# Performance work log

Measured on AMD Instinct MI355X. Metric: run time of the kernel, lower is better.

## Reference

```python
import jax, jax.numpy as jnp
import numpy as np

B, N, DIM = 4, 2048, 512
H, DH = 8, 64  # heads, dim_head; inner_dim = H*DH = 512


def setup_inputs() -> dict:
    key = jax.random.key(0)
    ks = jax.random.split(key, 7)
    s = 0.02
    return {
        "x": jax.random.normal(ks[0], (B, N, DIM), dtype=jnp.float32),
        "w_qkv": jax.random.normal(ks[1], (DIM, 3 * H * DH), dtype=jnp.float32) * s,
        "b_qkv": jnp.zeros((3 * H * DH,), dtype=jnp.float32),
        "th1": jax.random.normal(ks[2], (H, H), dtype=jnp.float32) * (1.0 / H) + jnp.eye(H, dtype=jnp.float32),
        "th2": jax.random.normal(ks[3], (H, H), dtype=jnp.float32) * (1.0 / H) + jnp.eye(H, dtype=jnp.float32),
        "w_out": jax.random.normal(ks[4], (H * DH, DIM), dtype=jnp.float32) * s,
        "b_out": jnp.zeros((DIM,), dtype=jnp.float32),
    }


def reference(x, w_qkv, b_qkv, th1, th2, w_out, b_out):
    b, n, _ = x.shape
    scale = DH ** -0.5
    qkv = x @ w_qkv + b_qkv                       # [b, n, 3*H*DH]
    q, k, v = jnp.split(qkv, 3, axis=-1)
    to_heads = lambda t: t.reshape(b, n, H, DH).transpose(0, 2, 1, 3)  # b h n d
    q, k, v = to_heads(q), to_heads(k), to_heads(v)
    dots = jnp.einsum('bhnd,bhmd->bhnm', q, k) * scale   # [b, h, n, n]
    dots = jnp.einsum('gh,bhnm->bgnm', th1, dots)        # talking-heads pre-softmax (1x1 conv over heads)
    attn = jax.nn.softmax(dots, axis=-1)
    attn = jnp.einsum('gh,bhnm->bgnm', th2, attn)        # talking-heads post-softmax
    out = jnp.einsum('bhnm,bhmd->bhnd', attn, v)         # [b, h, n, d]
    out = out.transpose(0, 2, 1, 3).reshape(b, n, H * DH)
    return out @ w_out + b_out
```

## Files before the change

kernel.cpp:

```cpp
#include <hip/hip_runtime.h>

typedef _Float16 half8  __attribute__((ext_vector_type(8)));
typedef _Float16 half4  __attribute__((ext_vector_type(4)));
typedef float    f32x4  __attribute__((ext_vector_type(4)));

#define MFMA32(a,b,c) __builtin_amdgcn_mfma_f32_16x16x32_f16(a,b,c,0,0,0)
#define MFMA16(a,b,c) __builtin_amdgcn_mfma_f32_16x16x16f16(a,b,c,0,0,0)

#if __has_builtin(__builtin_amdgcn_exp2f)
#define EXP2F(x) __builtin_amdgcn_exp2f(x)
#else
#define EXP2F(x) exp2f(x)
#endif

#define GLOAD16(gp, lp) __builtin_amdgcn_global_load_lds(                      \
    (const __attribute__((address_space(1))) void*)(gp),                       \
    (__attribute__((address_space(3))) void*)(lp), 16, 0, 0)

static constexpr float SCALE_LOG2E = 0.18033688011112042f;

static constexpr size_t QH_OFF = 0;
static constexpr size_t KH_OFF = (size_t)8  << 20;
static constexpr size_t VT_OFF = (size_t)16 << 20;
static constexpr size_t LS_OFF = (size_t)24 << 20;
static constexpr size_t O_OFF  = (size_t)25 << 20;
static constexpr size_t LPART  = (size_t)4*8*2048;
static constexpr size_t OPART  = (size_t)8192*512;

__global__ __launch_bounds__(256)
void k_qkv(const float* __restrict__ x, const float* __restrict__ w,
           const float* __restrict__ bias, _Float16* __restrict__ Qh,
           _Float16* __restrict__ Kh, _Float16* __restrict__ Vt)
{
  __shared__ __align__(16) _Float16 Xs[64*40];
  __shared__ __align__(16) _Float16 Wt[64*40];
  const int tid = threadIdx.x;
  const int wv = tid >> 6, lane = tid & 63, l15 = lane & 15, qd = lane >> 4;
  const int row0 = blockIdx.x * 64, col0 = blockIdx.y * 64;

  const int xr = tid >> 2, xc = (tid & 3) * 8;
  const int wk = tid >> 3, wc = (tid & 7) * 8;

  f32x4 acc[4] = {{0.f,0.f,0.f,0.f},{0.f,0.f,0.f,0.f},{0.f,0.f,0.f,0.f},{0.f,0.f,0.f,0.f}};

  for (int k0 = 0; k0 < 512; k0 += 32) {
    f32x4 a0 = *(const f32x4*)(x + (size_t)(row0 + xr) * 512 + k0 + xc);
    f32x4 a1 = *(const f32x4*)(x + (size_t)(row0 + xr) * 512 + k0 + xc + 4);
    f32x4 b0 = *(const f32x4*)(w + (size_t)(k0 + wk) * 1536 + col0 + wc);
    f32x4 b1 = *(const f32x4*)(w + (size_t)(k0 + wk) * 1536 + col0 + wc + 4);
    half8 hx;
#pragma unroll
    for (int j = 0; j < 4; j++) { hx[j] = (_Float16)a0[j]; hx[j+4] = (_Float16)a1[j]; }
    *(half8*)&Xs[xr*40 + xc] = hx;
#pragma unroll
    for (int j = 0; j < 4; j++) {
      Wt[(wc+j  )*40 + wk] = (_Float16)b0[j];
      Wt[(wc+j+4)*40 + wk] = (_Float16)b1[j];
    }
    __syncthreads();
    half8 af = *(const half8*)&Xs[(wv*16 + l15)*40 + qd*8];
#pragma unroll
    for (int ct = 0; ct < 4; ct++) {
      half8 bf = *(const half8*)&Wt[(ct*16 + l15)*40 + qd*8];
      acc[ct] = MFMA32(af, bf, acc[ct]);
    }
    __syncthreads();
  }
#pragma unroll
  for (int ct = 0; ct < 4; ct++) {
    const int c = col0 + ct*16 + l15;
    const int sec = c >> 9, hh = (c >> 6) & 7, d = c & 63;
    const float bv = bias[c];
#pragma unroll
    for (int i = 0; i < 4; i++) {
      const int row = row0 + wv*16 + qd*4 + i;
      const int bb = row >> 11, n = row & 2047;
      float v = acc[ct][i] + bv;
      if (sec == 0)
        Qh[((size_t)((bb*8 + hh)*2048 + n))*64 + d] = (_Float16)(v * SCALE_LOG2E);
      else if (sec == 1)
        Kh[((size_t)((bb*8 + hh)*2048 + n))*64 + d] = (_Float16)v;
      else
        Vt[((size_t)((bb*8 + hh)*64 + d))*2048 + n] = (_Float16)v;
    }
  }
}

__global__ __launch_bounds__(512, 4)
void k_pass1(const _Float16* __restrict__ Qh, const _Float16* __restrict__ Kh,
             const float* __restrict__ th1, float* __restrict__ Lsum)
{
  __shared__ __align__(16) _Float16 KB[8][1024];
  __shared__ __align__(16) _Float16 Sb[2][2][2592];
  const int tid = threadIdx.x;
  const int wv = tid >> 6, lane = tid & 63, l15 = lane & 15, qd = lane >> 4;
  const int s = blockIdx.x & 7, nt = blockIdx.x >> 3;
  const int b = s >> 1, mh = s & 1;
  const int n0 = nt << 5;
  const _Float16* kbase = Kh + ((size_t)((b*8 + wv)*2048 + mh*1024))*64;

  half4 a1f;
#pragma unroll
  for (int j = 0; j < 4; j++)
    a1f[j] = ((l15 >> 3) == (qd >> 1)) ? (_Float16)th1[(l15 & 7)*8 + (qd & 1)*4 + j]
                                       : (_Float16)0.f;

  half8 qf[2][2];
#pragma unroll
  for (int t = 0; t < 2; t++) {
    const _Float16* qp = Qh + ((size_t)((b*8 + wv)*2048 + n0 + t*16 + l15))*64 + qd*8;
    qf[t][0] = *(const half8*)qp;
    qf[t][1] = *(const half8*)(qp + 32);
  }

  auto issueK = [&](int it) {
#pragma unroll
    for (int j = 0; j < 2; j++) {
      const int bk = j*64 + lane;
      const int m = bk >> 3, c = bk & 7;
      const int cp = c ^ (m & 7);
      GLOAD16(kbase + (size_t)(it*16 + m)*64 + cp*8, &KB[wv][j*512]);
    }
  };
  auto qk_to_sb = [&](int buf) {
    half8 ka0 = *(const half8*)&KB[wv][l15*64 + ((qd       ^ (l15 & 7))*8)];
    half8 ka1 = *(const half8*)&KB[wv][l15*64 + (((4 + qd) ^ (l15 & 7))*8)];
#pragma unroll
    for (int t = 0; t < 2; t++) {
      f32x4 a = {0.f,0.f,0.f,0.f};
      a = MFMA32(ka0, qf[t][0], a);
      a = MFMA32(ka1, qf[t][1], a);
#pragma unroll
      for (int i = 0; i < 4; i++)
        Sb[buf][t][(l15 >> 1)*324 + (qd*4 + i)*20 + wv + 8*(l15 & 1)] = (_Float16)a[i];
    }
  };

  float lacc[2][4];
#pragma unroll
  for (int t = 0; t < 2; t++)
#pragma unroll
    for (int i = 0; i < 4; i++) lacc[t][i] = 0.f;

  issueK(0);
  __syncthreads();
  for (int it = 0; it <= 64; it++) {
    if (it < 64) {
      qk_to_sb(it & 1);
      if (it + 1 < 64) issueK(it + 1);
    }
    if (it >= 1) {
      const int buf = (it - 1) & 1;
#pragma unroll
      for (int t = 0; t < 2; t++) {
        half4 b1 = *(const half4*)&Sb[buf][t][wv*324 + l15*20 + qd*4];
        f32x4 c1 = MFMA16(a1f, b1, ((f32x4){0.f,0.f,0.f,0.f}));
#pragma unroll
        for (int i = 0; i < 4; i++) lacc[t][i] += EXP2F(c1[i]);
      }
    }
    __syncthreads();
  }

#pragma unroll
  for (int t = 0; t < 2; t++)
#pragma unroll
    for (int i = 0; i < 4; i++) {
      float v = lacc[t][i];
      v += __shfl_xor(v, 1); v += __shfl_xor(v, 2);
      v += __shfl_xor(v, 4); v += __shfl_xor(v, 8);
      lacc[t][i] = v;
    }
  if (l15 == 0) {
#pragma unroll
    for (int t = 0; t < 2; t++)
#pragma unroll
      for (int i = 0; i < 4; i++) {
        const int n = n0 + t*16 + wv*2 + (qd >> 1);
        const int g = (qd & 1)*4 + i;
        Lsum[(size_t)mh*LPART + (size_t)(b*8 + g)*2048 + n] = lacc[t][i];
      }
  }
}

__global__ __launch_bounds__(512, 4)
void k_pass2(const _Float16* __restrict__ Qh, const _Float16* __restrict__ Kh,
             const _Float16* __restrict__ Vt, const float* __restrict__ Lsum,
             const float* __restrict__ th1, const float* __restrict__ th2,
             _Float16* __restrict__ Obuf)
{
  __shared__ __align__(16) _Float16 KB[8][1024];
  __shared__ __align__(16) _Float16 VB[8][1024];
  __shared__ __align__(16) _Float16 Sb[2][2][2592];
  __shared__ __align__(16) _Float16 Wb[2][2][2592];
  const int tid = threadIdx.x;
  const int wv = tid >> 6, lane = tid & 63, l15 = lane & 15, qd = lane >> 4;
  const int s = blockIdx.x & 7, nt = blockIdx.x >> 3;
  const int b = s >> 1, mh = s & 1;
  const int n0 = nt << 5;
  const _Float16* kbase = Kh + ((size_t)((b*8 + wv)*2048 + mh*1024))*64;
  const _Float16* vbase = Vt + (size_t)(b*8 + wv)*64*2048 + mh*1024;

  half4 a1f, b2f;
#pragma unroll
  for (int j = 0; j < 4; j++) {
    const bool diag = ((l15 >> 3) == (qd >> 1));
    a1f[j] = diag ? (_Float16)th1[(l15 & 7)*8 + (qd & 1)*4 + j] : (_Float16)0.f;
    b2f[j] = diag ? (_Float16)th2[(l15 & 7)*8 + (qd & 1)*4 + j] : (_Float16)0.f;
  }

  f32x4 cs[2];
#pragma unroll
  for (int t = 0; t < 2; t++)
#pragma unroll
    for (int i = 0; i < 4; i++) {
      const int n = n0 + t*16 + wv*2 + (qd >> 1);
      const int g = (qd & 1)*4 + i;
      const size_t off = (size_t)(b*8 + g)*2048 + n;
      cs[t][i] = -__log2f(Lsum[off] + Lsum[off + LPART]);
    }

  half8 qf[2][2];
#pragma unroll
  for (int t = 0; t < 2; t++) {
    const _Float16* qp = Qh + ((size_t)((b*8 + wv)*2048 + n0 + t*16 + l15))*64 + qd*8;
    qf[t][0] = *(const half8*)qp;
    qf[t][1] = *(const half8*)(qp + 32);
  }

  auto issueK = [&](int it) {
#pragma unroll
    for (int j = 0; j < 2; j++) {
      const int bk = j*64 + lane;
      const int m = bk >> 3, c = bk & 7;
      const int cp = c ^ (m & 7);
      GLOAD16(kbase + (size_t)(it*16 + m)*64 + cp*8, &KB[wv][j*512]);
    }
  };
  auto issueV = [&](int it) {
#pragma unroll
    for (int j = 0; j < 2; j++) {
      const int bk = j*64 + lane;
      const int d = bk >> 1, c = bk & 1;
      const int cp = c ^ ((d >> 2) & 1);
      GLOAD16(vbase + (size_t)d*2048 + it*16 + cp*8, &VB[wv][j*512]);
    }
  };
  auto qk_to_sb = [&](int buf) {
    half8 ka0 = *(const half8*)&KB[wv][l15*64 + ((qd       ^ (l15 & 7))*8)];
    half8 ka1 = *(const half8*)&KB[wv][l15*64 + (((4 + qd) ^ (l15 & 7))*8)];
#pragma unroll
    for (int t = 0; t < 2; t++) {
      f32x4 a = {0.f,0.f,0.f,0.f};
      a = MFMA32(ka0, qf[t][0], a);
      a = MFMA32(ka1, qf[t][1], a);
#pragma unroll
      for (int i = 0; i < 4; i++)
        Sb[buf][t][(l15 >> 1)*324 + (qd*4 + i)*20 + wv + 8*(l15 & 1)] = (_Float16)a[i];
    }
  };

  f32x4 og[2][4];
#pragma unroll
  for (int t = 0; t < 2; t++)
#pragma unroll
    for (int dt = 0; dt < 4; dt++)
      og[t][dt] = (f32x4){0.f,0.f,0.f,0.f};

  issueK(0);
  __syncthreads();

  for (int it = 0; it <= 65; it++) {
    if (it < 64) {
      qk_to_sb(it & 1);
      if (it + 1 < 64) issueK(it + 1);
    }
    if (it >= 1 && it <= 64) {
      const int buf = (it - 1) & 1;
#pragma unroll
      for (int t = 0; t < 2; t++) {
        half4 b1 = *(const half4*)&Sb[buf][t][wv*324 + l15*20 + qd*4];
        f32x4 c1 = MFMA16(a1f, b1, cs[t]);
        half4 a2;
#pragma unroll
        for (int i = 0; i < 4; i++) a2[i] = (_Float16)EXP2F(c1[i]);
        f32x4 c2 = MFMA16(a2, b2f, ((f32x4){0.f,0.f,0.f,0.f}));
        half4 w4;
#pragma unroll
        for (int i = 0; i < 4; i++) w4[i] = (_Float16)c2[i];
        *(half4*)&Wb[buf][t][(l15 & 7)*324 + (wv*2 + (l15 >> 3))*20 + qd*4] = w4;
      }
    }
    if (it >= 2) {
      const int buf = (it - 2) & 1;
      half4 vb[4];
#pragma unroll
      for (int dt = 0; dt < 4; dt++) {
        const int rv = dt*16 + l15;
        vb[dt] = *(const half4*)&VB[wv][rv*16 +
                  (((qd >> 1) ^ ((rv >> 2) & 1))*8) + (qd & 1)*4];
      }
#pragma unroll
      for (int t = 0; t < 2; t++) {
        half4 af = *(const half4*)&Wb[buf][t][wv*324 + l15*20 + qd*4];
#pragma unroll
        for (int dt = 0; dt < 4; dt++)
          og[t][dt] = MFMA16(af, vb[dt], og[t][dt]);
      }
    }
    if (it >= 1 && it <= 64) issueV(it - 1);
    __syncthreads();
  }

  _Float16* Op = Obuf + (size_t)mh * OPART + ((size_t)(b*2048 + n0))*512;
#pragma unroll
  for (int t = 0; t < 2; t++)
#pragma unroll
    for (int dt = 0; dt < 4; dt++)
#pragma unroll
      for (int i = 0; i < 4; i++)
        Op[(size_t)(t*16 + qd*4 + i)*512 + wv*64 + dt*16 + l15] = (_Float16)og[t][dt][i];
}

__global__ __launch_bounds__(256)
void k_oproj(const _Float16* __restrict__ Ob, const float* __restrict__ w,
             const float* __restrict__ bias, float* __restrict__ out)
{
  __shared__ __align__(16) _Float16 Xs[64*40];
  __shared__ __align__(16) _Float16 Wt[64*40];
  const int tid = threadIdx.x;
  const int wv = tid >> 6, lane = tid & 63, l15 = lane & 15, qd = lane >> 4;
  const int row0 = blockIdx.x * 64, col0 = blockIdx.y * 64;
  const int xr = tid >> 2, xc = (tid & 3) * 8;
  const int wk = tid >> 3, wc = (tid & 7) * 8;

  f32x4 acc[4] = {{0.f,0.f,0.f,0.f},{0.f,0.f,0.f,0.f},{0.f,0.f,0.f,0.f},{0.f,0.f,0.f,0.f}};

  for (int k0 = 0; k0 < 512; k0 += 32) {
    const size_t idx = (size_t)(row0 + xr)*512 + k0 + xc;
    half8 a0 = *(const half8*)(Ob + idx);
    half8 a1 = *(const half8*)(Ob + OPART + idx);
    *(half8*)&Xs[xr*40 + xc] = a0 + a1;
    f32x4 b0 = *(const f32x4*)(w + (size_t)(k0 + wk)*512 + col0 + wc);
    f32x4 b1 = *(const f32x4*)(w + (size_t)(k0 + wk)*512 + col0 + wc + 4);
#pragma unroll
    for (int j = 0; j < 4; j++) {
      Wt[(wc+j  )*40 + wk] = (_Float16)b0[j];
      Wt[(wc+j+4)*40 + wk] = (_Float16)b1[j];
    }
    __syncthreads();
    half8 af = *(const half8*)&Xs[(wv*16 + l15)*40 + qd*8];
#pragma unroll
    for (int ct = 0; ct < 4; ct++) {
      half8 bf = *(const half8*)&Wt[(ct*16 + l15)*40 + qd*8];
      acc[ct] = MFMA32(af, bf, acc[ct]);
    }
    __syncthreads();
  }
#pragma unroll
  for (int ct = 0; ct < 4; ct++) {
    const int c = col0 + ct*16 + l15;
    const float bv = bias[c];
#pragma unroll
    for (int i = 0; i < 4; i++) {
      const int row = row0 + wv*16 + qd*4 + i;
      out[(size_t)row*512 + c] = acc[ct][i] + bv;
    }
  }
}

extern "C" void kernel_launch(void* const* d_in, const int* in_sizes, int n_in,
                              void* d_out, int out_size, void* d_ws, size_t ws_size,
                              hipStream_t stream)
{
  (void)in_sizes; (void)n_in; (void)out_size;
  const float* x     = (const float*)d_in[0];
  const float* w_qkv = (const float*)d_in[1];
  const float* b_qkv = (const float*)d_in[2];
  const float* th1   = (const float*)d_in[3];
  const float* th2   = (const float*)d_in[4];
  const float* w_out = (const float*)d_in[5];
  const float* b_out = (const float*)d_in[6];
  float* out = (float*)d_out;

  char* ws = (char*)d_ws;
  _Float16* Qh   = (_Float16*)(ws + QH_OFF);
  _Float16* Kh   = (_Float16*)(ws + KH_OFF);
  _Float16* Vt   = (_Float16*)(ws + VT_OFF);
  float*    Lsum = (float*)   (ws + LS_OFF);
  _Float16* Obuf = (_Float16*)(ws + O_OFF);
  if (ws_size < ((size_t)41 << 20)) return;

  k_qkv  <<<dim3(128, 24), 256, 0, stream>>>(x, w_qkv, b_qkv, Qh, Kh, Vt);
  k_pass1<<<dim3(512),     512, 0, stream>>>(Qh, Kh, th1, Lsum);
  k_pass2<<<dim3(512),     512, 0, stream>>>(Qh, Kh, Vt, Lsum, th1, th2, Obuf);
  k_oproj<<<dim3(128, 8),  256, 0, stream>>>(Obuf, w_out, b_out, out);
}
```

Before: 351.9 us.

## Pre-convert x and transposed W to fp16 and stage QKV GEMM via async LDS loads

Adds two small kernels that convert x to fp16 and transpose-convert w_qkv to fp16. The QKV GEMM then loads its tiles with global_load_lds into XOR-swizzled shared memory instead of converting fp32 in registers, which removes the scalar transposed shared-memory stores. Separately, the attention kernels change the S/W staging stride from 324 to 340 and use a simpler unswizzled V tile layout. This adds two launches and extra global traffic for the converted copies, and the new stride and V layout may change bank-conflict behaviour.

```diff
diff --git a/kernel.cpp b/kernel.cpp
--- a/kernel.cpp
+++ b/kernel.cpp
@@ -27,41 +27,61 @@
 static constexpr size_t LPART  = (size_t)4*8*2048;
 static constexpr size_t OPART  = (size_t)8192*512;
 
+static constexpr int GS = 340;
+
 __global__ __launch_bounds__(256)
-void k_qkv(const float* __restrict__ x, const float* __restrict__ w,
+void k_cvtx(const float* __restrict__ x, _Float16* __restrict__ xf)
+{
+  const size_t i = ((size_t)blockIdx.x*256 + threadIdx.x)*4;
+  f32x4 v = *(const f32x4*)(x + i);
+  half4 h;
+#pragma unroll
+  for (int j = 0; j < 4; j++) h[j] = (_Float16)v[j];
+  *(half4*)(xf + i) = h;
+}
+
+__global__ __launch_bounds__(256)
+void k_cvtw(const float* __restrict__ w, _Float16* __restrict__ wt)
+{
+  __shared__ _Float16 T[32][36];
+  const int kt = blockIdx.x, ct = blockIdx.y;
+  const int r = threadIdx.x >> 3, c4 = (threadIdx.x & 7)*4;
+  f32x4 v = *(const f32x4*)(w + (size_t)(kt*32 + r)*1536 + ct*32 + c4);
+#pragma unroll
+  for (int j = 0; j < 4; j++) T[r][c4 + j] = (_Float16)v[j];
+  __syncthreads();
+  half4 o;
+#pragma unroll
+  for (int j = 0; j < 4; j++) o[j] = T[c4 + j][r];
+  *(half4*)(wt + (size_t)(ct*32 + r)*512 + kt*32 + c4) = o;
+}
+
+__global__ __launch_bounds__(256)
+void k_qkv(const _Float16* __restrict__ xf, const _Float16* __restrict__ wt,
            const float* __restrict__ bias, _Float16* __restrict__ Qh,
            _Float16* __restrict__ Kh, _Float16* __restrict__ Vt)
 {
-  __shared__ __align__(16) _Float16 Xs[64*40];
-  __shared__ __align__(16) _Float16 Wt[64*40];
+  __shared__ __align__(16) _Float16 Xs[2048];
+  __shared__ __align__(16) _Float16 Ws[2048];
   const int tid = threadIdx.x;
   const int wv = tid >> 6, lane = tid & 63, l15 = lane & 15, qd = lane >> 4;
   const int row0 = blockIdx.x * 64, col0 = blockIdx.y * 64;
 
-  const int xr = tid >> 2, xc = (tid & 3) * 8;
-  const int wk = tid >> 3, wc = (tid & 7) * 8;
+  const int sslot = wv*64 + lane;
+  const int sr = sslot >> 2, so = (sslot & 3) ^ ((sr >> 1) & 3);
 
   f32x4 acc[4] = {{0.f,0.f,0.f,0.f},{0.f,0.f,0.f,0.f},{0.f,0.f,0.f,0.f},{0.f,0.f,0.f,0.f}};
 
   for (int k0 = 0; k0 < 512; k0 += 32) {
-    f32x4 a0 = *(const f32x4*)(x + (size_t)(row0 + xr) * 512 + k0 + xc);
-    f32x4 a1 = *(const f32x4*)(x + (size_t)(row0 + xr) * 512 + k0 + xc + 4);
-    f32x4 b0 = *(const f32x4*)(w + (size_t)(k0 + wk) * 1536 + col0 + wc);
-    f32x4 b1 = *(const f32x4*)(w + (size_t)(k0 + wk) * 1536 + col0 + wc + 4);
-    half8 hx;
-#pragma unroll
-    for (int j = 0; j < 4; j++) { hx[j] = (_Float16)a0[j]; hx[j+4] = (_Float16)a1[j]; }
-    *(half8*)&Xs[xr*40 + xc] = hx;
-#pragma unroll
-    for (int j = 0; j < 4; j++) {
-      Wt[(wc+j  )*40 + wk] = (_Float16)b0[j];
-      Wt[(wc+j+4)*40 + wk] = (_Float16)b1[j];
-    }
-    __syncthreads();
-    half8 af = *(const half8*)&Xs[(wv*16 + l15)*40 + qd*8];
+    GLOAD16(xf + (size_t)(row0 + sr)*512 + k0 + so*8, &Xs[wv*512]);
+    GLOAD16(wt + (size_t)(col0 + sr)*512 + k0 + so*8, &Ws[wv*512]);
+    __syncthreads();
+    const int ra = wv*16 + l15;
+    half8 af = *(const half8*)&Xs[(ra*4 + (qd ^ ((ra >> 1) & 3)))*8];
 #pragma unroll
     for (int ct = 0; ct < 4; ct++) {
-      half8 bf = *(const half8*)&Wt[(ct*16 + l15)*40 + qd*8];
+      const int rb = ct*16 + l15;
+      half8 bf = *(const half8*)&Ws[(rb*4 + (qd ^ ((rb >> 1) & 3)))*8];
       acc[ct] = MFMA32(af, bf, acc[ct]);
     }
     __syncthreads();
@@ -91,7 +111,7 @@
              const float* __restrict__ th1, float* __restrict__ Lsum)
 {
   __shared__ __align__(16) _Float16 KB[8][1024];
-  __shared__ __align__(16) _Float16 Sb[2][2][2592];
+  __shared__ __align__(16) _Float16 Sb[2][2][2704];
   const int tid = threadIdx.x;
   const int wv = tid >> 6, lane = tid & 63, l15 = lane & 15, qd = lane >> 4;
   const int s = blockIdx.x & 7, nt = blockIdx.x >> 3;
@@ -132,7 +152,7 @@
       a = MFMA32(ka1, qf[t][1], a);
 #pragma unroll
       for (int i = 0; i < 4; i++)
-        Sb[buf][t][(l15 >> 1)*324 + (qd*4 + i)*20 + wv + 8*(l15 & 1)] = (_Float16)a[i];
+        Sb[buf][t][(l15 >> 1)*GS + (qd*4 + i)*20 + wv + 8*(l15 & 1)] = (_Float16)a[i];
     }
   };
 
@@ -153,7 +173,7 @@
       const int buf = (it - 1) & 1;
 #pragma unroll
       for (int t = 0; t < 2; t++) {
-        half4 b1 = *(const half4*)&Sb[buf][t][wv*324 + l15*20 + qd*4];
+        half4 b1 = *(const half4*)&Sb[buf][t][wv*GS + l15*20 + qd*4];
         f32x4 c1 = MFMA16(a1f, b1, ((f32x4){0.f,0.f,0.f,0.f}));
 #pragma unroll
         for (int i = 0; i < 4; i++) lacc[t][i] += EXP2F(c1[i]);
@@ -191,8 +211,8 @@
 {
   __shared__ __align__(16) _Float16 KB[8][1024];
   __shared__ __align__(16) _Float16 VB[8][1024];
-  __shared__ __align__(16) _Float16 Sb[2][2][2592];
-  __shared__ __align__(16) _Float16 Wb[2][2][2592];
+  __shared__ __align__(16) _Float16 Sb[2][2][2704];
+  __shared__ __align__(16) _Float16 Wb[2][2][2704];
   const int tid = threadIdx.x;
   const int wv = tid >> 6, lane = tid & 63, l15 = lane & 15, qd = lane >> 4;
   const int s = blockIdx.x & 7, nt = blockIdx.x >> 3;
@@ -239,12 +259,8 @@
   };
   auto issueV = [&](int it) {
 #pragma unroll
-    for (int j = 0; j < 2; j++) {
-      const int bk = j*64 + lane;
-      const int d = bk >> 1, c = bk & 1;
-      const int cp = c ^ ((d >> 2) & 1);
-      GLOAD16(vbase + (size_t)d*2048 + it*16 + cp*8, &VB[wv][j*512]);
-    }
+    for (int j = 0; j < 2; j++)
+      GLOAD16(vbase + (size_t)lane*2048 + it*16 + j*8, &VB[wv][j*512]);
   };
   auto qk_to_sb = [&](int buf) {
     half8 ka0 = *(const half8*)&KB[wv][l15*64 + ((qd       ^ (l15 & 7))*8)];
@@ -256,7 +272,7 @@
       a = MFMA32(ka1, qf[t][1], a);
 #pragma unroll
       for (int i = 0; i < 4; i++)
-        Sb[buf][t][(l15 >> 1)*324 + (qd*4 + i)*20 + wv + 8*(l15 & 1)] = (_Float16)a[i];
+        Sb[buf][t][(l15 >> 1)*GS + (qd*4 + i)*20 + wv + 8*(l15 & 1)] = (_Float16)a[i];
     }
   };
 
@@ -279,7 +295,7 @@
       const int buf = (it - 1) & 1;
 #pragma unroll
       for (int t = 0; t < 2; t++) {
-        half4 b1 = *(const half4*)&Sb[buf][t][wv*324 + l15*20 + qd*4];
+        half4 b1 = *(const half4*)&Sb[buf][t][wv*GS + l15*20 + qd*4];
         f32x4 c1 = MFMA16(a1f, b1, cs[t]);
         half4 a2;
 #pragma unroll
@@ -288,21 +304,18 @@
         half4 w4;
 #pragma unroll
         for (int i = 0; i < 4; i++) w4[i] = (_Float16)c2[i];
-        *(half4*)&Wb[buf][t][(l15 & 7)*324 + (wv*2 + (l15 >> 3))*20 + qd*4] = w4;
+        *(half4*)&Wb[buf][t][(l15 & 7)*GS + (wv*2 + (l15 >> 3))*20 + qd*4] = w4;
       }
     }
     if (it >= 2) {
       const int buf = (it - 2) & 1;
       half4 vb[4];
 #pragma unroll
-      for (int dt = 0; dt < 4; dt++) {
-        const int rv = dt*16 + l15;
-        vb[dt] = *(const half4*)&VB[wv][rv*16 +
-                  (((qd >> 1) ^ ((rv >> 2) & 1))*8) + (qd & 1)*4];
-      }
+      for (int dt = 0; dt < 4; dt++)
+        vb[dt] = *(const half4*)&VB[wv][((qd >> 1)*64 + dt*16 + l15)*8 + (qd & 1)*4];
 #pragma unroll
       for (int t = 0; t < 2; t++) {
-        half4 af = *(const half4*)&Wb[buf][t][wv*324 + l15*20 + qd*4];
+        half4 af = *(const half4*)&Wb[buf][t][wv*GS + l15*20 + qd*4];
 #pragma unroll
         for (int dt = 0; dt < 4; dt++)
           og[t][dt] = MFMA16(af, vb[dt], og[t][dt]);
@@ -389,9 +402,13 @@
   _Float16* Vt   = (_Float16*)(ws + VT_OFF);
   float*    Lsum = (float*)   (ws + LS_OFF);
   _Float16* Obuf = (_Float16*)(ws + O_OFF);
+  _Float16* Xf   = (_Float16*)(ws + O_OFF);
+  _Float16* Wtf  = (_Float16*)(ws + O_OFF + ((size_t)8 << 20));
   if (ws_size < ((size_t)41 << 20)) return;
 
-  k_qkv  <<<dim3(128, 24), 256, 0, stream>>>(x, w_qkv, b_qkv, Qh, Kh, Vt);
+  k_cvtx <<<dim3(4096),    256, 0, stream>>>(x, Xf);
+  k_cvtw <<<dim3(16, 48),  256, 0, stream>>>(w_qkv, Wtf);
+  k_qkv  <<<dim3(128, 24), 256, 0, stream>>>(Xf, Wtf, b_qkv, Qh, Kh, Vt);
   k_pass1<<<dim3(512),     512, 0, stream>>>(Qh, Kh, th1, Lsum);
   k_pass2<<<dim3(512),     512, 0, stream>>>(Qh, Kh, Vt, Lsum, th1, th2, Obuf);
   k_oproj<<<dim3(128, 8),  256, 0, stream>>>(Obuf, w_out, b_out, out);
```

After: 324.9 us. -7.7%, faster.
